# Performance work log

Measured on AMD Instinct MI355X. Metric: run time of the kernel, lower is better.

Reference implementation:

```python
import jax, jax.numpy as jnp
import numpy as np

R_MIN = 0.1
R_MAX = 2.0

B, N, K = 8, 8192, 100  # batch, atoms, max neighbors


def setup_inputs() -> dict:
    key = jax.random.key(0)
    k1, k2, k3, k4, k5 = jax.random.split(key, 5)
    positions = jax.random.normal(k1, (B, N, 3), dtype=jnp.float32)
    cell = jax.random.normal(k2, (B, 3, 3), dtype=jnp.float32)
    offsets = jax.random.normal(k3, (B, N, K, 3), dtype=jnp.float32)
    neighbors = jax.random.randint(k4, (B, N, K), 0, N, dtype=jnp.int64)
    mask = jax.random.randint(k5, (B, N, K), 0, 2, dtype=jnp.int32)
    return {"positions": positions, "cell": cell, "offsets": offsets,
            "neighbors": neighbors, "mask": mask}


def reference(positions, cell, offsets, neighbors, mask):
    # gather neighbor positions: [B, N, K, 3]
    pos_j = jax.vmap(lambda p, n: p[n])(positions, neighbors)
    # fractional offsets -> cartesian: offsets @ cell per batch
    pos_j = pos_j + jnp.einsum('bnkd,bdc->bnkc', offsets, cell)
    vec = pos_j - positions[:, :, None, :]          # [B, N, K, 3]
    sq = jnp.sum(vec * vec, axis=-1)                # [B, N, K]
    valid = mask > 0
    sq_safe = jnp.where(valid, sq, 1.0)
    d = jnp.where(valid, jnp.sqrt(sq_safe), 0.0)    # masked distances = 0
    # f = 1/d^2, zeroed where d < r_min or d > r_max (masked entries have d=0 < r_min)
    keep = (d >= R_MIN) & (d <= R_MAX)
    f = jnp.where(keep, 1.0 / sq_safe, 0.0)
    return jnp.sum(f, axis=(1, 2)) * 0.5            # [B]
```

## Files before the change

kernel.cpp:

```cpp
#include <hip/hip_runtime.h>
#include <hip/hip_fp16.h>

typedef int            __attribute__((ext_vector_type(4))) i32x4;
typedef float          __attribute__((ext_vector_type(4))) f32x4;
typedef unsigned int   __attribute__((ext_vector_type(2))) u32x2;

constexpr int B_ = 8;
constexpr int N_ = 8192;
constexpr int K_ = 100;
constexpr int PER_BATCH = N_ * K_;
constexpr int QUADS_PER_BATCH = PER_BATCH / 4;
constexpr int THREADS = 1024;
constexpr int BLOCKS_PER_BATCH = 64;
constexpr int GRID = B_ * BLOCKS_PER_BATCH;
constexpr int QUADS_PER_BLOCK = QUADS_PER_BATCH / BLOCKS_PER_BATCH;
constexpr int FULL_ITERS = QUADS_PER_BLOCK / THREADS;
constexpr int TAIL = QUADS_PER_BLOCK - FULL_ITERS * THREADS;

constexpr float RMIN2 = 0.01f;
constexpr float RMAX2 = 4.0f;

__device__ __forceinline__ u32x2 pack_pos(float x, float y, float z) {
    const unsigned hx = __half_as_ushort(__float2half_rn(x));
    const unsigned hy = __half_as_ushort(__float2half_rn(y));
    const unsigned hz = __half_as_ushort(__float2half_rn(z));
    u32x2 r; r.x = hx | (hy << 16); r.y = hz;
    return r;
}

__global__ __launch_bounds__(THREADS, 2)
void repulsive_prior_kernel(const float* __restrict__ positions,
                            const float* __restrict__ cell,
                            const float* __restrict__ offsets,
                            const int*   __restrict__ neighbors,
                            const int*   __restrict__ mask,
                            float* __restrict__ out)
{
    __shared__ u32x2 spos[N_];
    __shared__ float wsum[THREADS / 64];

    const int bid   = blockIdx.x;
    const int b     = bid & 7;
    const int chunk = bid >> 3;
    const int t     = (int)threadIdx.x;

    const float* __restrict__ pos_b = positions + (size_t)b * N_ * 3;
    const float* __restrict__ off_b = offsets   + (size_t)b * PER_BATCH * 3;
    const int*   __restrict__ nb_b  = neighbors + (size_t)b * PER_BATCH;
    const int*   __restrict__ mk_b  = mask      + (size_t)b * PER_BATCH;

    const int qbase = chunk * QUADS_PER_BLOCK;
    auto qat = [&](int k) { return qbase + k * THREADS + t; };

    struct Quad { i32x4 nb, mk; f32x4 oa, ob, oc; };
    auto loadq = [&](int q) {
        Quad Q;
        Q.nb = *(const i32x4*)(nb_b  + 4 * (size_t)q);
        Q.mk = *(const i32x4*)(mk_b  + 4 * (size_t)q);
        Q.oa = *(const f32x4*)(off_b + 12 * (size_t)q);
        Q.ob = *(const f32x4*)(off_b + 12 * (size_t)q + 4);
        Q.oc = *(const f32x4*)(off_b + 12 * (size_t)q + 8);
        return Q;
    };

    Quad Q0 = loadq(qat(0));

    #pragma unroll
    for (int g0 = 0; g0 < 2; ++g0) {
        const int g = g0 * THREADS + t;
        const f32x4 v0 = *(const f32x4*)(pos_b + 12 * (size_t)g);
        const f32x4 v1 = *(const f32x4*)(pos_b + 12 * (size_t)g + 4);
        const f32x4 v2 = *(const f32x4*)(pos_b + 12 * (size_t)g + 8);
        spos[4 * g + 0] = pack_pos(v0.x, v0.y, v0.z);
        spos[4 * g + 1] = pack_pos(v0.w, v1.x, v1.y);
        spos[4 * g + 2] = pack_pos(v1.z, v1.w, v2.x);
        spos[4 * g + 3] = pack_pos(v2.y, v2.z, v2.w);
    }
    __syncthreads();

    const float* cb = cell + b * 9;
    const float c00 = cb[0], c01 = cb[1], c02 = cb[2];
    const float c10 = cb[3], c11 = cb[4], c12 = cb[5];
    const float c20 = cb[6], c21 = cb[7], c22 = cb[8];

    auto ldpos = [&](int row, float& x, float& y, float& z) {
        const u32x2 v = spos[row];
        x = __half2float(__ushort_as_half((unsigned short)(v.x & 0xffffu)));
        y = __half2float(__ushort_as_half((unsigned short)(v.x >> 16)));
        z = __half2float(__ushort_as_half((unsigned short)(v.y & 0xffffu)));
    };

    float acc = 0.0f;
    auto computeq = [&](const Quad& Q, int q) {
        const int n = q / 25;
        float pix, piy, piz;
        ldpos(n, pix, piy, piz);
        auto elem = [&](int m, int j, float o0, float o1, float o2) {
            float pjx, pjy, pjz;
            ldpos(j, pjx, pjy, pjz);
            const float vx = pjx + o0 * c00 + o1 * c10 + o2 * c20 - pix;
            const float vy = pjy + o0 * c01 + o1 * c11 + o2 * c21 - piy;
            const float vz = pjz + o0 * c02 + o1 * c12 + o2 * c22 - piz;
            const float sq = vx * vx + vy * vy + vz * vz;
            const bool keep = (m > 0) & (sq >= RMIN2) & (sq <= RMAX2);
            acc += keep ? (1.0f / sq) : 0.0f;
        };
        elem(Q.mk.x, Q.nb.x, Q.oa.x, Q.oa.y, Q.oa.z);
        elem(Q.mk.y, Q.nb.y, Q.oa.w, Q.ob.x, Q.ob.y);
        elem(Q.mk.z, Q.nb.z, Q.ob.z, Q.ob.w, Q.oc.x);
        elem(Q.mk.w, Q.nb.w, Q.oc.y, Q.oc.z, Q.oc.w);
    };

    Quad Q1 = loadq(qat(1));
    computeq(Q0, qat(0));
    Quad Q2 = loadq(qat(2));
    computeq(Q1, qat(1));
    if (t < TAIL) {
        Quad QT = loadq(qat(3));
        computeq(Q2, qat(2));
        computeq(QT, qat(3));
    } else {
        computeq(Q2, qat(2));
    }

    #pragma unroll
    for (int off = 32; off > 0; off >>= 1)
        acc += __shfl_down(acc, off, 64);

    const int wave = t >> 6;
    const int lane = t & 63;
    if (lane == 0) wsum[wave] = acc;
    __syncthreads();
    if (t == 0) {
        float s = 0.0f;
        #pragma unroll
        for (int w = 0; w < THREADS / 64; ++w) s += wsum[w];
        atomicAdd(&out[b], 0.5f * s);
    }
}

extern "C" void kernel_launch(void* const* d_in, const int* in_sizes, int n_in,
                              void* d_out, int out_size, void* d_ws, size_t ws_size,
                              hipStream_t stream) {
    const float* positions = (const float*)d_in[0];
    const float* cell      = (const float*)d_in[1];
    const float* offsets   = (const float*)d_in[2];
    const int*   neighbors = (const int*)d_in[3];
    const int*   mask      = (const int*)d_in[4];
    float* out = (float*)d_out;

    (void)hipMemsetAsync(out, 0, out_size * sizeof(float), stream);

    repulsive_prior_kernel<<<GRID, THREADS, 0, stream>>>(
        positions, cell, offsets, neighbors, mask, out);
}
```

Before: 31.49 us.

## Stage neighbor indices into LDS via async global_load_lds double buffering

Neighbor indices are now copied straight into a double-buffered LDS tile with global_load_lds. Mask and offset loads for the next tile are issued while the current tile is computed. The grid is halved to 32 blocks per batch, so each block covers 6400 quads in three 2048-quad tiles plus a tail, and launch bounds drop to one block per CU to fit the larger LDS footprint. The goal is better overlap of memory traffic with compute and less register pressure from neighbor loads, at the cost of lower occupancy and added barriers.

```diff
diff --git a/kernel.cpp b/kernel.cpp
--- a/kernel.cpp
+++ b/kernel.cpp
@@ -1,9 +1,9 @@
 #include <hip/hip_runtime.h>
 #include <hip/hip_fp16.h>
 
-typedef int            __attribute__((ext_vector_type(4))) i32x4;
-typedef float          __attribute__((ext_vector_type(4))) f32x4;
-typedef unsigned int   __attribute__((ext_vector_type(2))) u32x2;
+typedef int          __attribute__((ext_vector_type(4))) i32x4;
+typedef float        __attribute__((ext_vector_type(4))) f32x4;
+typedef unsigned int __attribute__((ext_vector_type(2))) u32x2;
 
 constexpr int B_ = 8;
 constexpr int N_ = 8192;
@@ -11,11 +11,11 @@
 constexpr int PER_BATCH = N_ * K_;
 constexpr int QUADS_PER_BATCH = PER_BATCH / 4;
 constexpr int THREADS = 1024;
-constexpr int BLOCKS_PER_BATCH = 64;
+constexpr int BLOCKS_PER_BATCH = 32;
 constexpr int GRID = B_ * BLOCKS_PER_BATCH;
 constexpr int QUADS_PER_BLOCK = QUADS_PER_BATCH / BLOCKS_PER_BATCH;
-constexpr int FULL_ITERS = QUADS_PER_BLOCK / THREADS;
-constexpr int TAIL = QUADS_PER_BLOCK - FULL_ITERS * THREADS;
+constexpr int TILE = 2048;
+constexpr int TAILQ = QUADS_PER_BLOCK - 3 * TILE;
 
 constexpr float RMIN2 = 0.01f;
 constexpr float RMAX2 = 4.0f;
@@ -28,7 +28,7 @@
     return r;
 }
 
-__global__ __launch_bounds__(THREADS, 2)
+__global__ __launch_bounds__(THREADS, 1)
 void repulsive_prior_kernel(const float* __restrict__ positions,
                             const float* __restrict__ cell,
                             const float* __restrict__ offsets,
@@ -37,12 +37,15 @@
                             float* __restrict__ out)
 {
     __shared__ u32x2 spos[N_];
+    __shared__ i32x4 nbbuf[2][TILE];
     __shared__ float wsum[THREADS / 64];
 
     const int bid   = blockIdx.x;
     const int b     = bid & 7;
     const int chunk = bid >> 3;
     const int t     = (int)threadIdx.x;
+    const int wid   = t >> 6;
+    const int lane  = t & 63;
 
     const float* __restrict__ pos_b = positions + (size_t)b * N_ * 3;
     const float* __restrict__ off_b = offsets   + (size_t)b * PER_BATCH * 3;
@@ -50,20 +53,31 @@
     const int*   __restrict__ mk_b  = mask      + (size_t)b * PER_BATCH;
 
     const int qbase = chunk * QUADS_PER_BLOCK;
-    auto qat = [&](int k) { return qbase + k * THREADS + t; };
 
-    struct Quad { i32x4 nb, mk; f32x4 oa, ob, oc; };
-    auto loadq = [&](int q) {
-        Quad Q;
-        Q.nb = *(const i32x4*)(nb_b  + 4 * (size_t)q);
-        Q.mk = *(const i32x4*)(mk_b  + 4 * (size_t)q);
-        Q.oa = *(const f32x4*)(off_b + 12 * (size_t)q);
-        Q.ob = *(const f32x4*)(off_b + 12 * (size_t)q + 4);
-        Q.oc = *(const f32x4*)(off_b + 12 * (size_t)q + 8);
-        return Q;
+    auto dma_nb = [&](int bufidx, int q0, int nq) {
+        const int nchunks = nq >> 6;
+        for (int c = wid; c < nchunks; c += THREADS / 64) {
+            const int* src = nb_b + 4 * (size_t)(q0 + c * 64) + lane * 4;
+            __builtin_amdgcn_global_load_lds(
+                (const __attribute__((address_space(1))) unsigned int*)src,
+                (__attribute__((address_space(3))) unsigned int*)&nbbuf[bufidx][c * 64],
+                16, 0, 0);
+        }
     };
 
-    Quad Q0 = loadq(qat(0));
+    struct SQ { i32x4 mk; f32x4 oa, ob, oc; };
+    auto loadS = [&](int q) {
+        SQ s;
+        s.mk = *(const i32x4*)(mk_b  + 4 * (size_t)q);
+        s.oa = *(const f32x4*)(off_b + 12 * (size_t)q);
+        s.ob = *(const f32x4*)(off_b + 12 * (size_t)q + 4);
+        s.oc = *(const f32x4*)(off_b + 12 * (size_t)q + 8);
+        return s;
+    };
+
+    dma_nb(0, qbase, TILE);
+    SQ a0 = loadS(qbase + t);
+    SQ a1 = loadS(qbase + 1024 + t);
 
     #pragma unroll
     for (int g0 = 0; g0 < 2; ++g0) {
@@ -91,7 +105,7 @@
     };
 
     float acc = 0.0f;
-    auto computeq = [&](const Quad& Q, int q) {
+    auto computeq = [&](const SQ& Q, const i32x4 nb, int q) {
         const int n = q / 25;
         float pix, piy, piz;
         ldpos(n, pix, piy, piz);
@@ -105,31 +119,44 @@
             const bool keep = (m > 0) & (sq >= RMIN2) & (sq <= RMAX2);
             acc += keep ? (1.0f / sq) : 0.0f;
         };
-        elem(Q.mk.x, Q.nb.x, Q.oa.x, Q.oa.y, Q.oa.z);
-        elem(Q.mk.y, Q.nb.y, Q.oa.w, Q.ob.x, Q.ob.y);
-        elem(Q.mk.z, Q.nb.z, Q.ob.z, Q.ob.w, Q.oc.x);
-        elem(Q.mk.w, Q.nb.w, Q.oc.y, Q.oc.z, Q.oc.w);
+        elem(Q.mk.x, nb.x, Q.oa.x, Q.oa.y, Q.oa.z);
+        elem(Q.mk.y, nb.y, Q.oa.w, Q.ob.x, Q.ob.y);
+        elem(Q.mk.z, nb.z, Q.ob.z, Q.ob.w, Q.oc.x);
+        elem(Q.mk.w, nb.w, Q.oc.y, Q.oc.z, Q.oc.w);
     };
 
-    Quad Q1 = loadq(qat(1));
-    computeq(Q0, qat(0));
-    Quad Q2 = loadq(qat(2));
-    computeq(Q1, qat(1));
-    if (t < TAIL) {
-        Quad QT = loadq(qat(3));
-        computeq(Q2, qat(2));
-        computeq(QT, qat(3));
-    } else {
-        computeq(Q2, qat(2));
-    }
+    dma_nb(1, qbase + TILE, TILE);
+    SQ b0 = loadS(qbase + TILE + t);
+    SQ b1 = loadS(qbase + TILE + 1024 + t);
+    __builtin_amdgcn_sched_barrier(0);
+    computeq(a0, nbbuf[0][t],        qbase + t);
+    computeq(a1, nbbuf[0][1024 + t], qbase + 1024 + t);
+    __syncthreads();
+
+    dma_nb(0, qbase + 2 * TILE, TILE);
+    SQ e0 = loadS(qbase + 2 * TILE + t);
+    SQ e1 = loadS(qbase + 2 * TILE + 1024 + t);
+    __builtin_amdgcn_sched_barrier(0);
+    computeq(b0, nbbuf[1][t],        qbase + TILE + t);
+    computeq(b1, nbbuf[1][1024 + t], qbase + TILE + 1024 + t);
+    __syncthreads();
+
+    dma_nb(1, qbase + 3 * TILE, TAILQ);
+    SQ d0;
+    if (t < TAILQ) d0 = loadS(qbase + 3 * TILE + t);
+    __builtin_amdgcn_sched_barrier(0);
+    computeq(e0, nbbuf[0][t],        qbase + 2 * TILE + t);
+    computeq(e1, nbbuf[0][1024 + t], qbase + 2 * TILE + 1024 + t);
+    __syncthreads();
+
+    if (t < TAILQ)
+        computeq(d0, nbbuf[1][t], qbase + 3 * TILE + t);
 
     #pragma unroll
     for (int off = 32; off > 0; off >>= 1)
         acc += __shfl_down(acc, off, 64);
 
-    const int wave = t >> 6;
-    const int lane = t & 63;
-    if (lane == 0) wsum[wave] = acc;
+    if (lane == 0) wsum[wid] = acc;
     __syncthreads();
     if (t == 0) {
         float s = 0.0f;
```

Result: slower. 44.03 us (+39.8%).

## Stream neighbor tiles through double-buffered LDS via global_load_lds DMA

Applied to the files above, without the earlier changes.

Replaces the per-thread vector register loads of neighbors, mask and offsets with double-buffered LDS tiles. Each tile is filled by wave-level global_load_lds (direct global-to-LDS) copies while the previous tile is being computed. Blocks per batch drop from 64 to 32, so each block does the redundant fp16 position staging into LDS half as often. The cost is one block per CU (about 144KB of LDS), a barrier per tile, and reliance on the barrier also waiting for the asynchronous LDS DMA to finish.

```diff
diff --git a/kernel.cpp b/kernel.cpp
--- a/kernel.cpp
+++ b/kernel.cpp
@@ -1,21 +1,24 @@
 #include <hip/hip_runtime.h>
 #include <hip/hip_fp16.h>
 
-typedef int            __attribute__((ext_vector_type(4))) i32x4;
-typedef float          __attribute__((ext_vector_type(4))) f32x4;
-typedef unsigned int   __attribute__((ext_vector_type(2))) u32x2;
+typedef int          __attribute__((ext_vector_type(2))) i32x2;
+typedef float        __attribute__((ext_vector_type(2))) f32x2;
+typedef float        __attribute__((ext_vector_type(4))) f32x4;
+typedef unsigned int __attribute__((ext_vector_type(2))) u32x2;
 
 constexpr int B_ = 8;
 constexpr int N_ = 8192;
 constexpr int K_ = 100;
 constexpr int PER_BATCH = N_ * K_;
-constexpr int QUADS_PER_BATCH = PER_BATCH / 4;
 constexpr int THREADS = 1024;
-constexpr int BLOCKS_PER_BATCH = 64;
+constexpr int NWAVES = THREADS / 64;
+constexpr int BLOCKS_PER_BATCH = 32;
 constexpr int GRID = B_ * BLOCKS_PER_BATCH;
-constexpr int QUADS_PER_BLOCK = QUADS_PER_BATCH / BLOCKS_PER_BATCH;
-constexpr int FULL_ITERS = QUADS_PER_BLOCK / THREADS;
-constexpr int TAIL = QUADS_PER_BLOCK - FULL_ITERS * THREADS;
+constexpr int ELEMS_PER_BLOCK = PER_BATCH / BLOCKS_PER_BATCH;
+constexpr int TILE_E = 2048;
+constexpr int NFULL = 12;
+constexpr int TAIL_E = ELEMS_PER_BLOCK - NFULL * TILE_E;
+constexpr int NTILES = NFULL + 1;
 
 constexpr float RMIN2 = 0.01f;
 constexpr float RMAX2 = 4.0f;
@@ -28,7 +31,13 @@
     return r;
 }
 
-__global__ __launch_bounds__(THREADS, 2)
+struct StreamBuf {
+    int   nb[TILE_E];
+    int   mk[TILE_E];
+    float off[3 * TILE_E];
+};
+
+__global__ __launch_bounds__(THREADS, 1)
 void repulsive_prior_kernel(const float* __restrict__ positions,
                             const float* __restrict__ cell,
                             const float* __restrict__ offsets,
@@ -37,33 +46,48 @@
                             float* __restrict__ out)
 {
     __shared__ u32x2 spos[N_];
-    __shared__ float wsum[THREADS / 64];
+    __shared__ StreamBuf sbuf[2];
+    __shared__ float wsum[NWAVES];
 
     const int bid   = blockIdx.x;
     const int b     = bid & 7;
     const int chunk = bid >> 3;
     const int t     = (int)threadIdx.x;
+    const int wid   = t >> 6;
+    const int lane  = t & 63;
 
     const float* __restrict__ pos_b = positions + (size_t)b * N_ * 3;
     const float* __restrict__ off_b = offsets   + (size_t)b * PER_BATCH * 3;
     const int*   __restrict__ nb_b  = neighbors + (size_t)b * PER_BATCH;
     const int*   __restrict__ mk_b  = mask      + (size_t)b * PER_BATCH;
 
-    const int qbase = chunk * QUADS_PER_BLOCK;
-    auto qat = [&](int k) { return qbase + k * THREADS + t; };
+    const int Ebase0 = chunk * ELEMS_PER_BLOCK;
 
-    struct Quad { i32x4 nb, mk; f32x4 oa, ob, oc; };
-    auto loadq = [&](int q) {
-        Quad Q;
-        Q.nb = *(const i32x4*)(nb_b  + 4 * (size_t)q);
-        Q.mk = *(const i32x4*)(mk_b  + 4 * (size_t)q);
-        Q.oa = *(const f32x4*)(off_b + 12 * (size_t)q);
-        Q.ob = *(const f32x4*)(off_b + 12 * (size_t)q + 4);
-        Q.oc = *(const f32x4*)(off_b + 12 * (size_t)q + 8);
-        return Q;
+    auto dma = [&](int bi, int Eb, int ne) {
+        StreamBuf* sb = &sbuf[bi];
+        const int nbc   = ne >> 8;
+        const int total = 5 * nbc;
+        for (int c = wid; c < total; c += NWAVES) {
+            const int* gsrc;
+            int* ldst;
+            if (c < nbc) {
+                gsrc = nb_b + Eb + (c << 8);
+                ldst = &sb->nb[c << 8];
+            } else if (c < 2 * nbc) {
+                gsrc = mk_b + Eb + ((c - nbc) << 8);
+                ldst = &sb->mk[(c - nbc) << 8];
+            } else {
+                gsrc = (const int*)(off_b + 3 * (size_t)Eb) + ((c - 2 * nbc) << 8);
+                ldst = (int*)&sb->off[(c - 2 * nbc) << 8];
+            }
+            __builtin_amdgcn_global_load_lds(
+                (const __attribute__((address_space(1))) unsigned int*)(gsrc + lane * 4),
+                (__attribute__((address_space(3))) unsigned int*)ldst,
+                16, 0, 0);
+        }
     };
 
-    Quad Q0 = loadq(qat(0));
+    dma(0, Ebase0, TILE_E);
 
     #pragma unroll
     for (int g0 = 0; g0 < 2; ++g0) {
@@ -91,50 +115,51 @@
     };
 
     float acc = 0.0f;
-    auto computeq = [&](const Quad& Q, int q) {
-        const int n = q / 25;
-        float pix, piy, piz;
+    auto elem = [&](int Ei, int m, int j, float o0, float o1, float o2) {
+        const int n = Ei / 100;
+        float pix, piy, piz, pjx, pjy, pjz;
         ldpos(n, pix, piy, piz);
-        auto elem = [&](int m, int j, float o0, float o1, float o2) {
-            float pjx, pjy, pjz;
-            ldpos(j, pjx, pjy, pjz);
-            const float vx = pjx + o0 * c00 + o1 * c10 + o2 * c20 - pix;
-            const float vy = pjy + o0 * c01 + o1 * c11 + o2 * c21 - piy;
-            const float vz = pjz + o0 * c02 + o1 * c12 + o2 * c22 - piz;
-            const float sq = vx * vx + vy * vy + vz * vz;
-            const bool keep = (m > 0) & (sq >= RMIN2) & (sq <= RMAX2);
-            acc += keep ? (1.0f / sq) : 0.0f;
-        };
-        elem(Q.mk.x, Q.nb.x, Q.oa.x, Q.oa.y, Q.oa.z);
-        elem(Q.mk.y, Q.nb.y, Q.oa.w, Q.ob.x, Q.ob.y);
-        elem(Q.mk.z, Q.nb.z, Q.ob.z, Q.ob.w, Q.oc.x);
-        elem(Q.mk.w, Q.nb.w, Q.oc.y, Q.oc.z, Q.oc.w);
+        ldpos(j, pjx, pjy, pjz);
+        const float vx = pjx + o0 * c00 + o1 * c10 + o2 * c20 - pix;
+        const float vy = pjy + o0 * c01 + o1 * c11 + o2 * c21 - piy;
+        const float vz = pjz + o0 * c02 + o1 * c12 + o2 * c22 - piz;
+        const float sq = vx * vx + vy * vy + vz * vz;
+        const bool keep = (m > 0) & (sq >= RMIN2) & (sq <= RMAX2);
+        acc += keep ? (1.0f / sq) : 0.0f;
     };
 
-    Quad Q1 = loadq(qat(1));
-    computeq(Q0, qat(0));
-    Quad Q2 = loadq(qat(2));
-    computeq(Q1, qat(1));
-    if (t < TAIL) {
-        Quad QT = loadq(qat(3));
-        computeq(Q2, qat(2));
-        computeq(QT, qat(3));
-    } else {
-        computeq(Q2, qat(2));
+    #pragma unroll 1
+    for (int k = 0; k < NTILES; ++k) {
+        if (k < NTILES - 1)
+            dma((k + 1) & 1, Ebase0 + (k + 1) * TILE_E,
+                (k + 1 == NFULL) ? TAIL_E : TILE_E);
+
+        StreamBuf* sb = &sbuf[k & 1];
+        const int ne = (k == NFULL) ? TAIL_E : TILE_E;
+        const int e0 = 2 * t;
+        if (e0 < ne) {
+            const i32x2 nb2 = *(const i32x2*)&sb->nb[e0];
+            const i32x2 mk2 = *(const i32x2*)&sb->mk[e0];
+            const f32x2 o01 = *(const f32x2*)&sb->off[3 * e0];
+            const f32x2 o23 = *(const f32x2*)&sb->off[3 * e0 + 2];
+            const f32x2 o45 = *(const f32x2*)&sb->off[3 * e0 + 4];
+            const int Ei = Ebase0 + k * TILE_E + e0;
+            elem(Ei,     mk2.x, nb2.x, o01.x, o01.y, o23.x);
+            elem(Ei + 1, mk2.y, nb2.y, o23.y, o45.x, o45.y);
+        }
+        __syncthreads();
     }
 
     #pragma unroll
     for (int off = 32; off > 0; off >>= 1)
         acc += __shfl_down(acc, off, 64);
 
-    const int wave = t >> 6;
-    const int lane = t & 63;
-    if (lane == 0) wsum[wave] = acc;
+    if (lane == 0) wsum[wid] = acc;
     __syncthreads();
     if (t == 0) {
         float s = 0.0f;
         #pragma unroll
-        for (int w = 0; w < THREADS / 64; ++w) s += wsum[w];
+        for (int w = 0; w < NWAVES; ++w) s += wsum[w];
         atomicAdd(&out[b], 0.5f * s);
     }
 }
```

New measurement: 33.67 us. +6.9%, slower.
